# Kernel tuning notes

Measured on AMD Instinct MI355X. Metric: run time of the kernel, lower is better.

## Reference

```python
import jax, jax.numpy as jnp
import numpy as np
from jax import lax

DIM = 64
H1 = 1024
H2 = 1024
BATCH = 32768


def build_masks(dim, h1, h2):
    # Standard MADE masks with identity ordering and deterministic hidden degrees.
    deg_in = np.arange(dim)
    deg_h1 = np.arange(h1) % max(1, dim - 1)
    deg_h2 = np.arange(h2) % max(1, dim - 1)
    deg_out = np.concatenate([np.arange(dim), np.arange(dim)])  # (mu, log_sigma)
    M1 = (deg_h1[None, :] >= deg_in[:, None]).astype(np.float32)   # [dim, h1]
    M2 = (deg_h2[None, :] >= deg_h1[:, None]).astype(np.float32)   # [h1, h2]
    M3 = (deg_out[None, :] > deg_h2[:, None]).astype(np.float32)   # [h2, 2*dim]
    return jnp.asarray(M1), jnp.asarray(M2), jnp.asarray(M3)


def setup_inputs() -> dict:
    key = jax.random.key(0)
    ks = jax.random.split(key, 4)
    scale = 0.02
    u = jax.random.normal(ks[0], (BATCH, DIM), dtype=jnp.float32)
    W1 = jax.random.normal(ks[1], (DIM, H1), dtype=jnp.float32) * scale
    b1 = jnp.zeros((H1,), dtype=jnp.float32)
    W2 = jax.random.normal(ks[2], (H1, H2), dtype=jnp.float32) * scale
    b2 = jnp.zeros((H2,), dtype=jnp.float32)
    W3 = jax.random.normal(ks[3], (H2, 2 * DIM), dtype=jnp.float32) * scale
    b3 = jnp.zeros((2 * DIM,), dtype=jnp.float32)
    return {"u": u, "W1": W1, "b1": b1, "W2": W2, "b2": b2, "W3": W3, "b3": b3}


def reference(u, W1, b1, W2, b2, W3, b3):
    B, dim = u.shape
    M1, M2, M3 = build_masks(dim, W1.shape[1], W2.shape[1])

    def made(x):
        h = jax.nn.relu(x @ (W1 * M1) + b1)
        h = jax.nn.relu(h @ (W2 * M2) + b2)
        out = h @ (W3 * M3) + b3
        return out[:, :dim], out[:, dim:]  # mu, log_sigma

    def step(carry, t):
        x, logd = carry
        mu, log_sigma = made(x)
        x = x.at[:, t].set(u[:, t] * jnp.exp(log_sigma[:, t]) + mu[:, t])
        logd = logd + log_sigma[:, t]
        return (x, logd), None

    x0 = jnp.zeros_like(u)
    logd0 = jnp.zeros((B,), dtype=u.dtype)
    (x, logd), _ = lax.scan(step, (x0, logd0), jnp.arange(dim))
    return x, logd
```

## Files before the change

kernel.cpp:

```cpp
#include <hip/hip_runtime.h>
#include <hip/hip_bf16.h>
#include <stdint.h>

typedef __attribute__((ext_vector_type(8))) short bf16x8;
typedef __attribute__((ext_vector_type(4))) float f32x4;
typedef __attribute__((ext_vector_type(4))) unsigned int u32x4;

#define MFMA __builtin_amdgcn_mfma_f32_16x16x32_bf16

__device__ __forceinline__ int nc_of(int t) {
    return (t <= 16) ? ((17 * t + 31) >> 5) : ((t + 2) >> 1);
}
__device__ __forceinline__ int orig_of(int s) {
    int d, k;
    if (s < 272) { d = s / 17; k = s - 17 * d; }
    else { int s2 = s - 272; d = 16 + (s2 >> 4); k = s2 & 15; }
    return d + 63 * k;
}
__device__ __forceinline__ ushort f2bf(float v) {
    __hip_bfloat16 b = __float2bfloat16(v);
    return *reinterpret_cast<ushort*>(&b);
}

__global__ void prep_all(const float* __restrict__ W1, const float* __restrict__ W2,
                         const float* __restrict__ W3, const float* __restrict__ b1,
                         const float* __restrict__ b2,
                         ushort* __restrict__ W2f, ushort* __restrict__ W2g,
                         ushort* __restrict__ W1f, ushort* __restrict__ W3f,
                         float* __restrict__ b1s, float* __restrict__ b2s)
{
    int idx = blockIdx.x * 256 + threadIdx.x;
    if (idx < 63 * 32 * 512) {
        int d = idx >> 14, rem = idx & 16383;
        int kc = rem >> 9, r = rem & 511;
        if (kc < nc_of(d + 1)) {
            int off = 0;
            for (int tt = 1; tt <= d; ++tt) off += nc_of(tt);
            int lane = r >> 3, e = r & 7;
            int col = lane & 15, k = kc * 32 + (lane >> 4) * 8 + e;
            int goff = (d < 16) ? 17 * d : 16 * d + 16;
            W2f[(size_t)(off + kc) * 512 + r] =
                f2bf(W2[(size_t)orig_of(k) * 1024 + orig_of(goff + col)]);
        }
    }
    if (idx < 16 * 9 * 512) {
        int d = idx / 4608, rem = idx - d * 4608;
        int r = rem & 511, kc = rem >> 9;
        int lane = r >> 3, e = r & 7;
        int col = lane & 15, k = kc * 32 + (lane >> 4) * 8 + e;
        W2g[idx] = f2bf(W2[(size_t)orig_of(k) * 1024 + orig_of(17 * d + 16 + col)]);
    }
    if (idx < 63 * 2048) {
        int d = idx >> 11, rem = idx & 2047;
        int kc2 = rem >> 10, nt = (rem >> 9) & 1, r = rem & 511;
        int lane = r >> 3, e = r & 7;
        int col = lane & 15, k = kc2 * 32 + (lane >> 4) * 8 + e;
        int goff = (d < 16) ? 17 * d : 16 * d + 16;
        int gsz = (d < 16) ? 17 : 16;
        int uo = nt * 16 + col;
        float v = (uo < gsz) ? W1[(size_t)k * 1024 + orig_of(goff + uo)] : 0.f;
        W1f[idx] = f2bf(v);
    }
    if (idx < 63 * 8 * 512) {
        int d = idx >> 12, rem = idx & 4095;
        int cb = rem >> 9, r = rem & 511;
        int lane = r >> 3, e = r & 7;
        int n = lane & 15, k = (lane >> 4) * 8 + e;
        int goff = (d < 16) ? 17 * d : 16 * d + 16;
        int gsz = (d < 16) ? 17 : 16;
        float v = (k < gsz) ? W3[(size_t)orig_of(goff + k) * 128 + cb * 16 + n] : 0.f;
        W3f[idx] = f2bf(v);
    }
    if (idx < 1024) { int o = orig_of(idx); b1s[idx] = b1[o]; b2s[idx] = b2[o]; }
}

template<int NCH, bool T2>
__device__ __forceinline__ void phase_b(const ushort* __restrict__ w2p,
                                        const ushort* __restrict__ w2gp,
                                        const char* h1b, int r16, int q, int lane8,
                                        f32x4& o1, f32x4& o2)
{
    bf16x8 bb[NCH];
    #pragma unroll
    for (int kc = 0; kc < NCH; ++kc)
        bb[kc] = *(const bf16x8*)(w2p + kc * 512 + lane8);
    bf16x8 gg[T2 ? NCH : 1];
    if constexpr (T2) {
        #pragma unroll
        for (int kc = 0; kc < NCH; ++kc)
            gg[kc] = *(const bf16x8*)(w2gp + kc * 512 + lane8);
    }
    f32x4 ce = {0,0,0,0}, co = {0,0,0,0}, ge = {0,0,0,0}, go = {0,0,0,0};
    #pragma unroll
    for (int kc = 0; kc < NCH; ++kc) {
        int bo = (r16 * 2048 + kc * 64 + q * 16) ^ ((r16 & 7) << 4);
        bf16x8 af = *(const bf16x8*)(h1b + bo);
        if (kc & 1) co = MFMA(af, bb[kc], co, 0, 0, 0);
        else        ce = MFMA(af, bb[kc], ce, 0, 0, 0);
        if constexpr (T2) {
            if (kc & 1) go = MFMA(af, gg[kc], go, 0, 0, 0);
            else        ge = MFMA(af, gg[kc], ge, 0, 0, 0);
        }
    }
    o1 = ce + co;
    if constexpr (T2) o2 = ge + go;
}

__global__ __launch_bounds__(256, 1)
void maf_main(const float* __restrict__ U, const float* __restrict__ b3,
              const ushort* __restrict__ W2f, const ushort* __restrict__ W2g,
              const ushort* __restrict__ W1f, const ushort* __restrict__ W3f,
              const float* __restrict__ b1s, const float* __restrict__ b2s,
              float* __restrict__ out)
{
    extern __shared__ char smem[];
    const int tid = threadIdx.x;
    const int w = tid >> 6, lane = tid & 63;
    const int r16 = lane & 15, q = lane >> 4;
    const int lane8 = lane * 8;
    char*   h1b = smem + w * 32768;
    ushort* xbs = (ushort*)(smem + 131072 + w * 2304);
    ushort* h2s = (ushort*)(smem + 140288 + w * 1024);
    float*  lgd = (float*)(smem + 144384 + w * 64);
    const int grow0 = blockIdx.x * 64 + w * 16;

    {
        u32x4 z = {0u,0u,0u,0u};
        for (int i = lane; i < 2048; i += 64) *(u32x4*)(h1b + i * 16) = z;
        for (int i = lane; i < 576; i += 64) ((uint32_t*)xbs)[i] = 0u;
        for (int i = lane; i < 256; i += 64) ((uint32_t*)h2s)[i] = 0u;
        if (lane < 16) lgd[lane] = 0.f;
    }

    f32x4 am0={0,0,0,0},am1={0,0,0,0},am2={0,0,0,0},am3={0,0,0,0};
    f32x4 al0={0,0,0,0},al1={0,0,0,0},al2={0,0,0,0},al3={0,0,0,0};

    size_t w2off = 0;

    for (int t = 0; t < 64; ++t) {
        const int tt = t >> 4, oc = t & 15;
        const float b3mu = b3[t], b3ls = b3[64 + t];
        float uu[4] = {0.f, 0.f, 0.f, 0.f};
        if (r16 == oc) {
            #pragma unroll
            for (int e = 0; e < 4; ++e)
                uu[e] = U[(size_t)(grow0 + q * 4 + e) * 64 + t];
        }

        if (t > 0) {
            const int d = t - 1;
            const int goff = (d < 16) ? 17 * d : 16 * d + 16;

            {
                const ushort* w1p = W1f + (size_t)d * 2048 + lane8;
                bf16x8 wf00 = *(const bf16x8*)(w1p);
                bf16x8 wf10 = *(const bf16x8*)(w1p + 1024);
                bf16x8 xa0 = *(const bf16x8*)(xbs + r16 * 72 + q * 8);
                bf16x8 xa1 = *(const bf16x8*)(xbs + r16 * 72 + 32 + q * 8);
                f32x4 h = {0,0,0,0};
                h = MFMA(xa0, wf00, h, 0, 0, 0);
                h = MFMA(xa1, wf10, h, 0, 0, 0);
                float bb1 = b1s[goff + r16];
                #pragma unroll
                for (int e = 0; e < 4; ++e) {
                    int row = q * 4 + e;
                    ushort hv = f2bf(fmaxf(h[e] + bb1, 0.f));
                    int bo = (row * 2048 + (goff + r16) * 2) ^ ((row & 7) << 4);
                    *(ushort*)(h1b + bo) = hv;
                }
                if (d < 16) {
                    bf16x8 wf01 = *(const bf16x8*)(w1p + 512);
                    bf16x8 wf11 = *(const bf16x8*)(w1p + 1536);
                    f32x4 g = {0,0,0,0};
                    g = MFMA(xa0, wf01, g, 0, 0, 0);
                    g = MFMA(xa1, wf11, g, 0, 0, 0);
                    if (r16 == 0) {
                        float bb2 = b1s[goff + 16];
                        #pragma unroll
                        for (int e = 0; e < 4; ++e) {
                            int row = q * 4 + e;
                            ushort hv = f2bf(fmaxf(g[e] + bb2, 0.f));
                            int bo = (row * 2048 + (goff + 16) * 2) ^ ((row & 7) << 4);
                            *(ushort*)(h1b + bo) = hv;
                        }
                    }
                }
            }

            f32x4 o1, o2 = {0,0,0,0};
            const ushort* w2p = W2f + w2off;
            const ushort* w2gp = W2g + (size_t)d * 9 * 512;
            if (t <= 17) {
                if (d < 16) phase_b<9, true>(w2p, w2gp, h1b, r16, q, lane8, o1, o2);
                else        phase_b<9, false>(w2p, w2gp, h1b, r16, q, lane8, o1, o2);
            }
            else if (t <= 25) phase_b<13, false>(w2p, w2gp, h1b, r16, q, lane8, o1, o2);
            else if (t <= 33) phase_b<17, false>(w2p, w2gp, h1b, r16, q, lane8, o1, o2);
            else if (t <= 42) phase_b<22, false>(w2p, w2gp, h1b, r16, q, lane8, o1, o2);
            else if (t <= 52) phase_b<27, false>(w2p, w2gp, h1b, r16, q, lane8, o1, o2);
            else              phase_b<32, false>(w2p, w2gp, h1b, r16, q, lane8, o1, o2);
            w2off += (size_t)nc_of(t) * 512;

            {
                float bb2 = b2s[goff + r16];
                #pragma unroll
                for (int e = 0; e < 4; ++e) {
                    int row = q * 4 + e;
                    ushort hv = f2bf(fmaxf(o1[e] + bb2, 0.f));
                    int bo = (row * 64 + r16 * 2) ^ (e << 4);
                    *(ushort*)((char*)h2s + bo) = hv;
                }
                if (r16 == 0) {
                    float bb3 = (d < 16) ? b2s[goff + 16] : 0.f;
                    #pragma unroll
                    for (int e = 0; e < 4; ++e) {
                        int row = q * 4 + e;
                        ushort hv = (d < 16) ? f2bf(fmaxf(o2[e] + bb3, 0.f)) : (ushort)0;
                        int bo = (row * 64 + 32) ^ (e << 4);
                        *(ushort*)((char*)h2s + bo) = hv;
                    }
                }
            }

            {
                int abo = (r16 * 64 + q * 16) ^ ((r16 & 3) << 4);
                bf16x8 ha = *(const bf16x8*)((char*)h2s + abo);
                const ushort* w3p = W3f + (size_t)d * 4096 + lane8;
                bf16x8 f0 = *(const bf16x8*)(w3p);
                bf16x8 f1 = *(const bf16x8*)(w3p + 512);
                bf16x8 f2 = *(const bf16x8*)(w3p + 1024);
                bf16x8 f3 = *(const bf16x8*)(w3p + 1536);
                bf16x8 f4 = *(const bf16x8*)(w3p + 2048);
                bf16x8 f5 = *(const bf16x8*)(w3p + 2560);
                bf16x8 f6 = *(const bf16x8*)(w3p + 3072);
                bf16x8 f7 = *(const bf16x8*)(w3p + 3584);
                am0 = MFMA(ha, f0, am0, 0, 0, 0);
                am1 = MFMA(ha, f1, am1, 0, 0, 0);
                am2 = MFMA(ha, f2, am2, 0, 0, 0);
                am3 = MFMA(ha, f3, am3, 0, 0, 0);
                al0 = MFMA(ha, f4, al0, 0, 0, 0);
                al1 = MFMA(ha, f5, al1, 0, 0, 0);
                al2 = MFMA(ha, f6, al2, 0, 0, 0);
                al3 = MFMA(ha, f7, al3, 0, 0, 0);
            }
        }

        {
            f32x4 vm = (tt == 0) ? am0 : (tt == 1) ? am1 : (tt == 2) ? am2 : am3;
            f32x4 vl = (tt == 0) ? al0 : (tt == 1) ? al1 : (tt == 2) ? al2 : al3;
            if (r16 == oc) {
                #pragma unroll
                for (int e = 0; e < 4; ++e) {
                    int row = q * 4 + e;
                    float mu = vm[e] + b3mu;
                    float ls = vl[e] + b3ls;
                    float xv = uu[e] * expf(ls) + mu;
                    out[(size_t)(grow0 + row) * 64 + t] = xv;
                    xbs[row * 72 + t] = f2bf(xv);
                    lgd[row] += ls;
                }
            }
        }
    }

    if (lane < 16) out[(size_t)32768 * 64 + grow0 + lane] = lgd[lane];
}

extern "C" void kernel_launch(void* const* d_in, const int* in_sizes, int n_in,
                              void* d_out, int out_size, void* d_ws, size_t ws_size,
                              hipStream_t stream) {
    const float* U  = (const float*)d_in[0];
    const float* W1 = (const float*)d_in[1];
    const float* b1 = (const float*)d_in[2];
    const float* W2 = (const float*)d_in[3];
    const float* b2 = (const float*)d_in[4];
    const float* W3 = (const float*)d_in[5];
    const float* b3 = (const float*)d_in[6];
    float* out = (float*)d_out;

    char* ws = (char*)d_ws;
    ushort* W2f = (ushort*)ws;
    ushort* W2g = (ushort*)(ws + 1080320);
    ushort* W1f = (ushort*)(ws + 1227776);
    ushort* W3f = (ushort*)(ws + 1485824);
    float*  b1s = (float*)(ws + 2001920);
    float*  b2s = (float*)(ws + 2006016);

    prep_all<<<4032, 256, 0, stream>>>(W1, W2, W3, b1, b2, W2f, W2g, W1f, W3f, b1s, b2s);

    const int smem_bytes = 144640;
    hipFuncSetAttribute(reinterpret_cast<const void*>(&maf_main),
                        hipFuncAttributeMaxDynamicSharedMemorySize, smem_bytes);
    maf_main<<<512, 256, smem_bytes, stream>>>(U, b3, W2f, W2g, W1f, W3f, b1s, b2s, out);
}
```

Before: 351.1 us.

## Keep layer-1 activations in registers and shrink LDS to allow two blocks per CU

Layer-1 hidden activations now live as MFMA A-fragments in a 33-entry register array, filled each step through a small LDS staging tile, replacing the 32KB-per-wave LDS buffer. Shared memory falls from about 144KB to about 22KB, and launch bounds are raised to two blocks per CU. W2 gets a regular per-step layout of 32 interleaved chunks plus one extra-unit chunk, the bias arrays are split to match, and phase_b uses a four-deep rolling prefetch with four accumulators. The cost is high register pressure from the fragment array and the switch-based indexed write, which could spill. Fixed-size W2 slabs also replace the old variable-length packing, so some zero chunks are stored and the per-step chunk counts change.

```diff
diff --git a/kernel.cpp b/kernel.cpp
--- a/kernel.cpp
+++ b/kernel.cpp
@@ -8,15 +8,6 @@
 
 #define MFMA __builtin_amdgcn_mfma_f32_16x16x32_bf16
 
-__device__ __forceinline__ int nc_of(int t) {
-    return (t <= 16) ? ((17 * t + 31) >> 5) : ((t + 2) >> 1);
-}
-__device__ __forceinline__ int orig_of(int s) {
-    int d, k;
-    if (s < 272) { d = s / 17; k = s - 17 * d; }
-    else { int s2 = s - 272; d = 16 + (s2 >> 4); k = s2 & 15; }
-    return d + 63 * k;
-}
 __device__ __forceinline__ ushort f2bf(float v) {
     __hip_bfloat16 b = __float2bfloat16(v);
     return *reinterpret_cast<ushort*>(&b);
@@ -25,117 +16,148 @@
 __global__ void prep_all(const float* __restrict__ W1, const float* __restrict__ W2,
                          const float* __restrict__ W3, const float* __restrict__ b1,
                          const float* __restrict__ b2,
-                         ushort* __restrict__ W2f, ushort* __restrict__ W2g,
+                         ushort* __restrict__ W2f2, ushort* __restrict__ W2g2,
                          ushort* __restrict__ W1f, ushort* __restrict__ W3f,
-                         float* __restrict__ b1s, float* __restrict__ b2s)
+                         float* __restrict__ b1s2, float* __restrict__ b1e,
+                         float* __restrict__ b2s2, float* __restrict__ b2e)
 {
     int idx = blockIdx.x * 256 + threadIdx.x;
-    if (idx < 63 * 32 * 512) {
-        int d = idx >> 14, rem = idx & 16383;
+    if (idx < 63 * 33 * 512) {
+        int d = idx / (33 * 512); int rem = idx - d * 33 * 512;
         int kc = rem >> 9, r = rem & 511;
-        if (kc < nc_of(d + 1)) {
-            int off = 0;
-            for (int tt = 1; tt <= d; ++tt) off += nc_of(tt);
-            int lane = r >> 3, e = r & 7;
-            int col = lane & 15, k = kc * 32 + (lane >> 4) * 8 + e;
-            int goff = (d < 16) ? 17 * d : 16 * d + 16;
-            W2f[(size_t)(off + kc) * 512 + r] =
-                f2bf(W2[(size_t)orig_of(k) * 1024 + orig_of(goff + col)]);
-        }
+        int lane = r >> 3, e = r & 7;
+        int col = lane & 15, s = ((lane >> 4) << 3) + e;
+        int hout = d + 63 * col;
+        float v = 0.f;
+        if (kc < 32) {
+            int g = 2 * kc + (s >> 4), m = s & 15;
+            if (g <= 62) v = W2[(size_t)(g + 63 * m) * 1024 + hout];
+        } else if (s < 16) {
+            v = W2[(size_t)(1008 + s) * 1024 + hout];
+        }
+        W2f2[idx] = f2bf(v);
     }
     if (idx < 16 * 9 * 512) {
-        int d = idx / 4608, rem = idx - d * 4608;
-        int r = rem & 511, kc = rem >> 9;
+        int d = idx / (9 * 512); int rem = idx - d * 9 * 512;
+        int j = rem >> 9, r = rem & 511;
         int lane = r >> 3, e = r & 7;
-        int col = lane & 15, k = kc * 32 + (lane >> 4) * 8 + e;
-        W2g[idx] = f2bf(W2[(size_t)orig_of(k) * 1024 + orig_of(17 * d + 16 + col)]);
+        int col = lane & 15, s = ((lane >> 4) << 3) + e;
+        float v = 0.f;
+        if (col == 0) {
+            int hout = 1008 + d;
+            if (j < 8) {
+                int g = 2 * j + (s >> 4), m = s & 15;
+                if (g <= 62) v = W2[(size_t)(g + 63 * m) * 1024 + hout];
+            } else if (s < 16) {
+                v = W2[(size_t)(1008 + s) * 1024 + hout];
+            }
+        }
+        W2g2[idx] = f2bf(v);
     }
     if (idx < 63 * 2048) {
-        int d = idx >> 11, rem = idx & 2047;
+        int d = idx >> 11; int rem = idx & 2047;
         int kc2 = rem >> 10, nt = (rem >> 9) & 1, r = rem & 511;
         int lane = r >> 3, e = r & 7;
-        int col = lane & 15, k = kc2 * 32 + (lane >> 4) * 8 + e;
-        int goff = (d < 16) ? 17 * d : 16 * d + 16;
-        int gsz = (d < 16) ? 17 : 16;
-        int uo = nt * 16 + col;
-        float v = (uo < gsz) ? W1[(size_t)k * 1024 + orig_of(goff + uo)] : 0.f;
+        int col = lane & 15, k = kc2 * 32 + ((lane >> 4) << 3) + e;
+        float v = 0.f;
+        if (nt == 0) v = W1[(size_t)k * 1024 + d + 63 * col];
+        else if (d < 16 && col == 0) v = W1[(size_t)k * 1024 + 1008 + d];
         W1f[idx] = f2bf(v);
     }
     if (idx < 63 * 8 * 512) {
-        int d = idx >> 12, rem = idx & 4095;
+        int d = idx >> 12; int rem = idx & 4095;
         int cb = rem >> 9, r = rem & 511;
         int lane = r >> 3, e = r & 7;
-        int n = lane & 15, k = (lane >> 4) * 8 + e;
-        int goff = (d < 16) ? 17 * d : 16 * d + 16;
-        int gsz = (d < 16) ? 17 : 16;
-        float v = (k < gsz) ? W3[(size_t)orig_of(goff + k) * 128 + cb * 16 + n] : 0.f;
+        int ncol = lane & 15, s = ((lane >> 4) << 3) + e;
+        int c = cb * 16 + ncol;
+        float v = 0.f;
+        if (s < 16) v = W3[(size_t)(d + 63 * s) * 128 + c];
+        else if (s == 16 && d < 16) v = W3[(size_t)(1008 + d) * 128 + c];
         W3f[idx] = f2bf(v);
     }
-    if (idx < 1024) { int o = orig_of(idx); b1s[idx] = b1[o]; b2s[idx] = b2[o]; }
-}
-
-template<int NCH, bool T2>
-__device__ __forceinline__ void phase_b(const ushort* __restrict__ w2p,
-                                        const ushort* __restrict__ w2gp,
-                                        const char* h1b, int r16, int q, int lane8,
+    if (idx < 1008) {
+        int d = idx >> 4, m = idx & 15;
+        b1s2[idx] = b1[d + 63 * m];
+        b2s2[idx] = b2[d + 63 * m];
+    }
+    if (idx < 16) { b1e[idx] = b1[1008 + idx]; b2e[idx] = b2[1008 + idx]; }
+}
+
+template<int CM, bool T2>
+__device__ __forceinline__ void phase_b(const char* __restrict__ w2p,
+                                        const char* __restrict__ w2gp,
+                                        const bf16x8 (&h1f)[33], int lane16,
                                         f32x4& o1, f32x4& o2)
 {
-    bf16x8 bb[NCH];
+    constexpr int N = CM + 1;
+    constexpr int PF = (N < 4) ? N : 4;
+    bf16x8 bb[4]; bf16x8 gg[4];
     #pragma unroll
-    for (int kc = 0; kc < NCH; ++kc)
-        bb[kc] = *(const bf16x8*)(w2p + kc * 512 + lane8);
-    bf16x8 gg[T2 ? NCH : 1];
-    if constexpr (T2) {
-        #pragma unroll
-        for (int kc = 0; kc < NCH; ++kc)
-            gg[kc] = *(const bf16x8*)(w2gp + kc * 512 + lane8);
-    }
-    f32x4 ce = {0,0,0,0}, co = {0,0,0,0}, ge = {0,0,0,0}, go = {0,0,0,0};
+    for (int i = 0; i < PF; ++i) {
+        int kc = (i < CM) ? i : 32;
+        bb[i] = *(const bf16x8*)(w2p + kc * 1024 + lane16);
+        if constexpr (T2) gg[i] = *(const bf16x8*)(w2gp + i * 1024 + lane16);
+    }
+    f32x4 c0 = {0,0,0,0}, c1 = {0,0,0,0}, c2 = {0,0,0,0}, c3 = {0,0,0,0};
+    f32x4 g0 = {0,0,0,0}, g1 = {0,0,0,0};
     #pragma unroll
-    for (int kc = 0; kc < NCH; ++kc) {
-        int bo = (r16 * 2048 + kc * 64 + q * 16) ^ ((r16 & 7) << 4);
-        bf16x8 af = *(const bf16x8*)(h1b + bo);
-        if (kc & 1) co = MFMA(af, bb[kc], co, 0, 0, 0);
-        else        ce = MFMA(af, bb[kc], ce, 0, 0, 0);
+    for (int i = 0; i < N; ++i) {
+        int kc = (i < CM) ? i : 32;
+        bf16x8 a = h1f[kc];
+        bf16x8 b = bb[i & 3];
+        if ((i & 3) == 0)      c0 = MFMA(a, b, c0, 0, 0, 0);
+        else if ((i & 3) == 1) c1 = MFMA(a, b, c1, 0, 0, 0);
+        else if ((i & 3) == 2) c2 = MFMA(a, b, c2, 0, 0, 0);
+        else                   c3 = MFMA(a, b, c3, 0, 0, 0);
         if constexpr (T2) {
-            if (kc & 1) go = MFMA(af, gg[kc], go, 0, 0, 0);
-            else        ge = MFMA(af, gg[kc], ge, 0, 0, 0);
-        }
-    }
-    o1 = ce + co;
-    if constexpr (T2) o2 = ge + go;
-}
-
-__global__ __launch_bounds__(256, 1)
+            bf16x8 g = gg[i & 3];
+            if (i & 1) g1 = MFMA(a, g, g1, 0, 0, 0);
+            else       g0 = MFMA(a, g, g0, 0, 0, 0);
+        }
+        if (i + 4 < N) {
+            int kn = (i + 4 < CM) ? (i + 4) : 32;
+            bb[i & 3] = *(const bf16x8*)(w2p + kn * 1024 + lane16);
+            if constexpr (T2) gg[i & 3] = *(const bf16x8*)(w2gp + (i + 4) * 1024 + lane16);
+        }
+    }
+    o1 = (c0 + c1) + (c2 + c3);
+    if constexpr (T2) o2 = g0 + g1;
+}
+
+__global__ __launch_bounds__(256, 2)
 void maf_main(const float* __restrict__ U, const float* __restrict__ b3,
-              const ushort* __restrict__ W2f, const ushort* __restrict__ W2g,
+              const ushort* __restrict__ W2f2, const ushort* __restrict__ W2g2,
               const ushort* __restrict__ W1f, const ushort* __restrict__ W3f,
-              const float* __restrict__ b1s, const float* __restrict__ b2s,
+              const float* __restrict__ b1s2, const float* __restrict__ b1e,
+              const float* __restrict__ b2s2, const float* __restrict__ b2e,
               float* __restrict__ out)
 {
-    extern __shared__ char smem[];
+    __shared__ char smem[4*1024 + 4*1024 + 4*1024 + 4*2304 + 4*64];
     const int tid = threadIdx.x;
     const int w = tid >> 6, lane = tid & 63;
     const int r16 = lane & 15, q = lane >> 4;
-    const int lane8 = lane * 8;
-    char*   h1b = smem + w * 32768;
-    ushort* xbs = (ushort*)(smem + 131072 + w * 2304);
-    ushort* h2s = (ushort*)(smem + 140288 + w * 1024);
-    float*  lgd = (float*)(smem + 144384 + w * 64);
+    const int lane16 = lane << 4;
+    char*   stgm = smem + w * 1024;
+    char*   stge = smem + 4096 + w * 1024;
+    char*   h2s  = smem + 8192 + w * 1024;
+    ushort* xbs  = (ushort*)(smem + 12288 + w * 2304);
+    float*  lgd  = (float*)(smem + 21504 + w * 64);
     const int grow0 = blockIdx.x * 64 + w * 16;
 
     {
-        u32x4 z = {0u,0u,0u,0u};
-        for (int i = lane; i < 2048; i += 64) *(u32x4*)(h1b + i * 16) = z;
+        u32x4 z = {0u, 0u, 0u, 0u};
+        for (int i = lane; i < 64; i += 64) *(u32x4*)(stge + i * 16) = z;
+        for (int i = lane; i < 64; i += 64) *(u32x4*)(h2s + i * 16) = z;
         for (int i = lane; i < 576; i += 64) ((uint32_t*)xbs)[i] = 0u;
-        for (int i = lane; i < 256; i += 64) ((uint32_t*)h2s)[i] = 0u;
         if (lane < 16) lgd[lane] = 0.f;
     }
+
+    bf16x8 h1f[33];
+    #pragma unroll
+    for (int i = 0; i < 33; ++i) h1f[i] = (bf16x8){0,0,0,0,0,0,0,0};
 
     f32x4 am0={0,0,0,0},am1={0,0,0,0},am2={0,0,0,0},am3={0,0,0,0};
     f32x4 al0={0,0,0,0},al1={0,0,0,0},al2={0,0,0,0},al3={0,0,0,0};
-
-    size_t w2off = 0;
 
     for (int t = 0; t < 64; ++t) {
         const int tt = t >> 4, oc = t & 15;
@@ -149,91 +171,103 @@
 
         if (t > 0) {
             const int d = t - 1;
-            const int goff = (d < 16) ? 17 * d : 16 * d + 16;
+            const int jc = d >> 1;
 
             {
-                const ushort* w1p = W1f + (size_t)d * 2048 + lane8;
+                const char* w1p = (const char*)W1f + (size_t)d * 4096 + lane16;
                 bf16x8 wf00 = *(const bf16x8*)(w1p);
-                bf16x8 wf10 = *(const bf16x8*)(w1p + 1024);
+                bf16x8 wf10 = *(const bf16x8*)(w1p + 2048);
                 bf16x8 xa0 = *(const bf16x8*)(xbs + r16 * 72 + q * 8);
                 bf16x8 xa1 = *(const bf16x8*)(xbs + r16 * 72 + 32 + q * 8);
                 f32x4 h = {0,0,0,0};
                 h = MFMA(xa0, wf00, h, 0, 0, 0);
                 h = MFMA(xa1, wf10, h, 0, 0, 0);
-                float bb1 = b1s[goff + r16];
+                float bb1 = b1s2[d * 16 + r16];
                 #pragma unroll
                 for (int e = 0; e < 4; ++e) {
                     int row = q * 4 + e;
                     ushort hv = f2bf(fmaxf(h[e] + bb1, 0.f));
-                    int bo = (row * 2048 + (goff + r16) * 2) ^ ((row & 7) << 4);
-                    *(ushort*)(h1b + bo) = hv;
+                    *(ushort*)(stgm + ((row * 64 + ((d & 1) << 5) + r16 * 2) ^ ((row & 3) << 4))) = hv;
+                    if (!(d & 1))
+                        *(ushort*)(stgm + ((row * 64 + 32 + r16 * 2) ^ ((row & 3) << 4))) = 0;
                 }
                 if (d < 16) {
-                    bf16x8 wf01 = *(const bf16x8*)(w1p + 512);
-                    bf16x8 wf11 = *(const bf16x8*)(w1p + 1536);
+                    bf16x8 wf01 = *(const bf16x8*)(w1p + 1024);
+                    bf16x8 wf11 = *(const bf16x8*)(w1p + 3072);
                     f32x4 g = {0,0,0,0};
                     g = MFMA(xa0, wf01, g, 0, 0, 0);
                     g = MFMA(xa1, wf11, g, 0, 0, 0);
                     if (r16 == 0) {
-                        float bb2 = b1s[goff + 16];
+                        float be = b1e[d];
                         #pragma unroll
                         for (int e = 0; e < 4; ++e) {
                             int row = q * 4 + e;
-                            ushort hv = f2bf(fmaxf(g[e] + bb2, 0.f));
-                            int bo = (row * 2048 + (goff + 16) * 2) ^ ((row & 7) << 4);
-                            *(ushort*)(h1b + bo) = hv;
+                            ushort hv = f2bf(fmaxf(g[e] + be, 0.f));
+                            *(ushort*)(stge + ((row * 64 + d * 2) ^ ((row & 3) << 4))) = hv;
                         }
                     }
                 }
             }
+            {
+                bf16x8 nf = *(const bf16x8*)(stgm + ((r16 * 64 + q * 16) ^ ((r16 & 3) << 4)));
+                switch (jc) {
+                    case 0:  h1f[0]=nf;  break; case 1:  h1f[1]=nf;  break;
+                    case 2:  h1f[2]=nf;  break; case 3:  h1f[3]=nf;  break;
+                    case 4:  h1f[4]=nf;  break; case 5:  h1f[5]=nf;  break;
+                    case 6:  h1f[6]=nf;  break; case 7:  h1f[7]=nf;  break;
+                    case 8:  h1f[8]=nf;  break; case 9:  h1f[9]=nf;  break;
+                    case 10: h1f[10]=nf; break; case 11: h1f[11]=nf; break;
+                    case 12: h1f[12]=nf; break; case 13: h1f[13]=nf; break;
+                    case 14: h1f[14]=nf; break; case 15: h1f[15]=nf; break;
+                    case 16: h1f[16]=nf; break; case 17: h1f[17]=nf; break;
+                    case 18: h1f[18]=nf; break; case 19: h1f[19]=nf; break;
+                    case 20: h1f[20]=nf; break; case 21: h1f[21]=nf; break;
+                    case 22: h1f[22]=nf; break; case 23: h1f[23]=nf; break;
+                    case 24: h1f[24]=nf; break; case 25: h1f[25]=nf; break;
+                    case 26: h1f[26]=nf; break; case 27: h1f[27]=nf; break;
+                    case 28: h1f[28]=nf; break; case 29: h1f[29]=nf; break;
+                    case 30: h1f[30]=nf; break; default: h1f[31]=nf; break;
+                }
+                if (d < 16)
+                    h1f[32] = *(const bf16x8*)(stge + ((r16 * 64 + q * 16) ^ ((r16 & 3) << 4)));
+            }
 
             f32x4 o1, o2 = {0,0,0,0};
-            const ushort* w2p = W2f + w2off;
-            const ushort* w2gp = W2g + (size_t)d * 9 * 512;
-            if (t <= 17) {
-                if (d < 16) phase_b<9, true>(w2p, w2gp, h1b, r16, q, lane8, o1, o2);
-                else        phase_b<9, false>(w2p, w2gp, h1b, r16, q, lane8, o1, o2);
-            }
-            else if (t <= 25) phase_b<13, false>(w2p, w2gp, h1b, r16, q, lane8, o1, o2);
-            else if (t <= 33) phase_b<17, false>(w2p, w2gp, h1b, r16, q, lane8, o1, o2);
-            else if (t <= 42) phase_b<22, false>(w2p, w2gp, h1b, r16, q, lane8, o1, o2);
-            else if (t <= 52) phase_b<27, false>(w2p, w2gp, h1b, r16, q, lane8, o1, o2);
-            else              phase_b<32, false>(w2p, w2gp, h1b, r16, q, lane8, o1, o2);
-            w2off += (size_t)nc_of(t) * 512;
+            const char* w2p = (const char*)W2f2 + (size_t)d * 33 * 1024;
+            const char* w2gp = (const char*)W2g2 + (size_t)d * 9 * 1024;
+            if (t <= 16)      phase_b<8,  true >(w2p, w2gp, h1f, lane16, o1, o2);
+            else if (t <= 28) phase_b<14, false>(w2p, w2gp, h1f, lane16, o1, o2);
+            else if (t <= 40) phase_b<20, false>(w2p, w2gp, h1f, lane16, o1, o2);
+            else if (t <= 52) phase_b<26, false>(w2p, w2gp, h1f, lane16, o1, o2);
+            else              phase_b<32, false>(w2p, w2gp, h1f, lane16, o1, o2);
 
             {
-                float bb2 = b2s[goff + r16];
+                const char* w3p = (const char*)W3f + (size_t)d * 8192 + lane16;
+                bf16x8 f0 = *(const bf16x8*)(w3p);
+                bf16x8 f1 = *(const bf16x8*)(w3p + 1024);
+                bf16x8 f2 = *(const bf16x8*)(w3p + 2048);
+                bf16x8 f3 = *(const bf16x8*)(w3p + 3072);
+                bf16x8 f4 = *(const bf16x8*)(w3p + 4096);
+                bf16x8 f5 = *(const bf16x8*)(w3p + 5120);
+                bf16x8 f6 = *(const bf16x8*)(w3p + 6144);
+                bf16x8 f7 = *(const bf16x8*)(w3p + 7168);
+                float bb2 = b2s2[d * 16 + r16];
                 #pragma unroll
                 for (int e = 0; e < 4; ++e) {
                     int row = q * 4 + e;
                     ushort hv = f2bf(fmaxf(o1[e] + bb2, 0.f));
-                    int bo = (row * 64 + r16 * 2) ^ (e << 4);
-                    *(ushort*)((char*)h2s + bo) = hv;
+                    *(ushort*)(h2s + ((row * 64 + r16 * 2) ^ ((row & 3) << 4))) = hv;
                 }
                 if (r16 == 0) {
-                    float bb3 = (d < 16) ? b2s[goff + 16] : 0.f;
+                    float be2 = (d < 16) ? b2e[d] : 0.f;
                     #pragma unroll
                     for (int e = 0; e < 4; ++e) {
                         int row = q * 4 + e;
-                        ushort hv = (d < 16) ? f2bf(fmaxf(o2[e] + bb3, 0.f)) : (ushort)0;
-                        int bo = (row * 64 + 32) ^ (e << 4);
-                        *(ushort*)((char*)h2s + bo) = hv;
+                        ushort hv = (d < 16) ? f2bf(fmaxf(o2[e] + be2, 0.f)) : (ushort)0;
+                        *(ushort*)(h2s + ((row * 64 + 32) ^ ((row & 3) << 4))) = hv;
                     }
                 }
-            }
-
-            {
-                int abo = (r16 * 64 + q * 16) ^ ((r16 & 3) << 4);
-                bf16x8 ha = *(const bf16x8*)((char*)h2s + abo);
-                const ushort* w3p = W3f + (size_t)d * 4096 + lane8;
-                bf16x8 f0 = *(const bf16x8*)(w3p);
-                bf16x8 f1 = *(const bf16x8*)(w3p + 512);
-                bf16x8 f2 = *(const bf16x8*)(w3p + 1024);
-                bf16x8 f3 = *(const bf16x8*)(w3p + 1536);
-                bf16x8 f4 = *(const bf16x8*)(w3p + 2048);
-                bf16x8 f5 = *(const bf16x8*)(w3p + 2560);
-                bf16x8 f6 = *(const bf16x8*)(w3p + 3072);
-                bf16x8 f7 = *(const bf16x8*)(w3p + 3584);
+                bf16x8 ha = *(const bf16x8*)(h2s + ((r16 * 64 + q * 16) ^ ((r16 & 3) << 4)));
                 am0 = MFMA(ha, f0, am0, 0, 0, 0);
                 am1 = MFMA(ha, f1, am1, 0, 0, 0);
                 am2 = MFMA(ha, f2, am2, 0, 0, 0);
@@ -279,17 +313,17 @@
     float* out = (float*)d_out;
 
     char* ws = (char*)d_ws;
-    ushort* W2f = (ushort*)ws;
-    ushort* W2g = (ushort*)(ws + 1080320);
-    ushort* W1f = (ushort*)(ws + 1227776);
-    ushort* W3f = (ushort*)(ws + 1485824);
-    float*  b1s = (float*)(ws + 2001920);
-    float*  b2s = (float*)(ws + 2006016);
-
-    prep_all<<<4032, 256, 0, stream>>>(W1, W2, W3, b1, b2, W2f, W2g, W1f, W3f, b1s, b2s);
-
-    const int smem_bytes = 144640;
-    hipFuncSetAttribute(reinterpret_cast<const void*>(&maf_main),
-                        hipFuncAttributeMaxDynamicSharedMemorySize, smem_bytes);
-    maf_main<<<512, 256, smem_bytes, stream>>>(U, b3, W2f, W2g, W1f, W3f, b1s, b2s, out);
-}
+    ushort* W2f2 = (ushort*)ws;
+    ushort* W2g2 = (ushort*)(ws + 2128896);
+    ushort* W1f  = (ushort*)(ws + 2276352);
+    ushort* W3f  = (ushort*)(ws + 2534400);
+    float*  b1s2 = (float*)(ws + 3050496);
+    float*  b1e  = (float*)(ws + 3054592);
+    float*  b2s2 = (float*)(ws + 3054720);
+    float*  b2e  = (float*)(ws + 3058752);
+
+    prep_all<<<4160, 256, 0, stream>>>(W1, W2, W3, b1, b2,
+                                       W2f2, W2g2, W1f, W3f, b1s2, b1e, b2s2, b2e);
+    maf_main<<<512, 256, 0, stream>>>(U, b3, W2f2, W2g2, W1f, W3f,
+                                      b1s2, b1e, b2s2, b2e, out);
+}
```

Result: faster. 281.7 us (-19.7%).
